# Kernel optimization log

Measured on AMD Instinct MI355X. Metric: run time of the kernel, lower is better.

The kernel has to match this reference:

```python
import jax, jax.numpy as jnp
import numpy as np

NUM_ITER = 5  # num_iterations
M, N, B = 972, 1944, 8  # check_matrix_row, check_matrix_column, unit_batch_size
ROW_DEG = 8  # check-node degree of the sparse parity matrix


def setup_inputs() -> dict:
    key = jax.random.key(0)
    # sparse binary parity-check matrix H (constant Tanner graph)
    rng = np.random.default_rng(0)
    H = np.zeros((M, N), np.float32)
    for i in range(M):
        H[i, rng.choice(N, ROW_DEG, replace=False)] = 1.0
    soft_input = 2.0 * jax.random.normal(key, (B, N), dtype=jnp.float32)  # channel LLRs
    check_weight = jnp.array([-1.07], dtype=jnp.float32)  # NMS init constant
    return {"soft_input": soft_input, "H": jnp.asarray(H), "check_weight": check_weight}


def _bp_iteration(cv, soft_input, H, check_weight):
    # ---- compute_vc (NMS: bit weight == 1.0) ----
    total = jnp.sum(cv, axis=1) + soft_input              # [B, N]
    vc = total[:, None, :] * H - cv                       # [B, M, N]
    # ---- compute_cv (min-sum branch) ----
    back = jnp.where(H == 0, -1e30 - 1.0, 0.0)[None]      # mask non-edges
    a = jnp.clip(jnp.abs(vc), 0.0, 1e30)
    dec = -a + back
    top2, _ = jax.lax.top_k(dec, 2)                       # [B, M, 2]
    min1 = (-top2[..., 0])[:, :, None] * H                # row min broadcast on edges
    min2 = (-top2[..., 1])[:, :, None] * H                # row second-min
    result = jnp.where(a > min1, min1, min2)              # exclude-self min
    sign_info = (1.0 - H)[None] + vc
    s = jnp.sign(sign_info)
    tot_sign = jnp.prod(s, axis=2)[:, :, None] * H
    result_sign = tot_sign * s                            # exclude-self sign product
    w = jax.nn.softplus(check_weight)                     # scalar NMS factor
    cv_new = result * jax.lax.stop_gradient(result_sign) * w
    return cv_new


def reference(soft_input, H, check_weight):
    Bn, n = soft_input.shape
    m = H.shape[0]
    cv0 = jnp.zeros((Bn, m, n), dtype=soft_input.dtype)

    def body(cv, _):
        return _bp_iteration(cv, soft_input, H, check_weight), None

    cv, _ = jax.lax.scan(body, cv0, None, length=NUM_ITER)
    # marginalize
    soft_output = jnp.sum(cv, axis=1) + soft_input
    return soft_output
```

## Files before the change

### kernel.cpp

```cpp
#include <hip/hip_runtime.h>
#include <math.h>

#define MM 972
#define NN 1944
#define BB 8
#define RD 8
#define NITER 5
#define MAXD 20
#define NEDGE (MM * RD)
#define DUMMY NEDGE

__global__ void build_adj(const float* __restrict__ H,
                          int* __restrict__ col_cnt,
                          int* __restrict__ row_cols,
                          int* __restrict__ col_edges) {
    const int m = blockIdx.x;
    __shared__ int cnt;
    if (threadIdx.x == 0) cnt = 0;
    __syncthreads();
    for (int n = threadIdx.x; n < NN; n += blockDim.x) {
        if (H[m * NN + n] != 0.0f) {
            int j = atomicAdd(&cnt, 1);
            row_cols[m * RD + j] = n;
            int k = atomicAdd(&col_cnt[n], 1);
            if (k < MAXD) col_edges[n * MAXD + k] = m * RD + j;
        }
    }
}

__global__ __launch_bounds__(1024, 1) void decode(const float* __restrict__ soft,
                                                  const float* __restrict__ cwp,
                                                  const int* __restrict__ col_cnt,
                                                  const int* __restrict__ row_cols,
                                                  const int* __restrict__ col_edges,
                                                  float* __restrict__ out) {
    __shared__ float cv_lds[NEDGE + 8];
    __shared__ float tot[NN];

    const int b = blockIdx.x;
    const int t = threadIdx.x;
    const float* soft_b = soft + b * NN;

    const float w = log1pf(expf(cwp[0]));

    const int n0 = t;
    const int n1 = t + 1024;
    const bool has1 = (n1 < NN);
    const float s0 = soft_b[n0];
    const float s1 = has1 ? soft_b[n1] : 0.0f;

    int e0[MAXD], e1[MAXD];
    {
        const int d0 = min(col_cnt[n0], MAXD);
        const int d1 = has1 ? min(col_cnt[n1], MAXD) : 0;
#pragma unroll
        for (int k = 0; k < MAXD; ++k) {
            e0[k] = (k < d0) ? col_edges[n0 * MAXD + k] : DUMMY;
            e1[k] = (k < d1) ? col_edges[n1 * MAXD + k] : DUMMY;
        }
    }

    int rc[RD];
    float cv[RD];
    if (t < MM) {
#pragma unroll
        for (int j = 0; j < RD; ++j) {
            rc[j] = row_cols[t * RD + j];
            cv[j] = 0.0f;
        }
    }

    tot[n0] = s0;
    if (has1) tot[n1] = s1;
    if (t == 0) {
#pragma unroll
        for (int k = 0; k < 8; ++k) cv_lds[NEDGE + k] = 0.0f;
    }
    __syncthreads();

    for (int it = 0; it < NITER; ++it) {
        if (t < MM) {
            float v[RD];
            float m1 = 3.0e38f, m2 = 3.0e38f, p = 1.0f;
#pragma unroll
            for (int j = 0; j < RD; ++j) {
                float vv = tot[rc[j]] - cv[j];
                v[j] = vv;
                float a = fminf(fabsf(vv), 1.0e30f);
                float s = (vv > 0.0f) ? 1.0f : ((vv < 0.0f) ? -1.0f : 0.0f);
                p *= s;
                if (a < m1) { m2 = m1; m1 = a; }
                else if (a < m2) { m2 = a; }
            }
#pragma unroll
            for (int j = 0; j < RD; ++j) {
                float a = fminf(fabsf(v[j]), 1.0e30f);
                float mag = (a > m1) ? m1 : m2;
                float s = (v[j] > 0.0f) ? 1.0f : ((v[j] < 0.0f) ? -1.0f : 0.0f);
                float nc = mag * (p * s) * w;
                cv[j] = nc;
                cv_lds[t * RD + j] = nc;
            }
        }
        __syncthreads();

        float a0 = 0.0f, a1 = 0.0f;
#pragma unroll
        for (int k = 0; k < MAXD; ++k) {
            a0 += cv_lds[e0[k]];
            a1 += cv_lds[e1[k]];
        }
        const float t0 = s0 + a0;
        const float t1 = s1 + a1;
        if (it == NITER - 1) {
            out[b * NN + n0] = t0;
            if (has1) out[b * NN + n1] = t1;
        } else {
            tot[n0] = t0;
            if (has1) tot[n1] = t1;
            __syncthreads();
        }
    }
}

extern "C" void kernel_launch(void* const* d_in, const int* in_sizes, int n_in,
                              void* d_out, int out_size, void* d_ws, size_t ws_size,
                              hipStream_t stream) {
    const float* soft = (const float*)d_in[0];
    const float* H    = (const float*)d_in[1];
    const float* cw   = (const float*)d_in[2];
    float* out = (float*)d_out;

    int* col_cnt   = (int*)d_ws;
    int* row_cols  = col_cnt + NN;
    int* col_edges = row_cols + MM * RD;

    hipMemsetAsync(col_cnt, 0, NN * sizeof(int), stream);
    build_adj<<<MM, 256, 0, stream>>>(H, col_cnt, row_cols, col_edges);
    decode<<<BB, 1024, 0, stream>>>(soft, cw, col_cnt, row_cols, col_edges, out);
}
```

Baseline: 87.04 us.

## Store check-to-variable messages in column-major padded slots for float4 gathers

Check nodes now scatter their messages into per-column slots (16 per variable node, with a rotating swizzle), so variable nodes sum their incoming messages with four float4 LDS loads instead of twenty scalar indexed gathers. This drops the per-column edge-index registers and the dummy-padded gather. The memset is replaced by a small zeroing kernel. LDS use grows to about 124 KB, and the scheme assumes column degree stays at or below 16; extra edges would collide in the last slot.

```diff
diff --git a/kernel.cpp b/kernel.cpp
--- a/kernel.cpp
+++ b/kernel.cpp
@@ -6,14 +6,17 @@
 #define BB 8
 #define RD 8
 #define NITER 5
-#define MAXD 20
-#define NEDGE (MM * RD)
-#define DUMMY NEDGE
+#define MAXD 16
+
+__global__ void zero_cnt(int* __restrict__ c) {
+    int i = blockIdx.x * blockDim.x + threadIdx.x;
+    if (i < NN) c[i] = 0;
+}
 
 __global__ void build_adj(const float* __restrict__ H,
                           int* __restrict__ col_cnt,
                           int* __restrict__ row_cols,
-                          int* __restrict__ col_edges) {
+                          int* __restrict__ row_slots) {
     const int m = blockIdx.x;
     __shared__ int cnt;
     if (threadIdx.x == 0) cnt = 0;
@@ -21,20 +24,21 @@
     for (int n = threadIdx.x; n < NN; n += blockDim.x) {
         if (H[m * NN + n] != 0.0f) {
             int j = atomicAdd(&cnt, 1);
-            row_cols[m * RD + j] = n;
             int k = atomicAdd(&col_cnt[n], 1);
-            if (k < MAXD) col_edges[n * MAXD + k] = m * RD + j;
+            if (k > MAXD - 1) k = MAXD - 1;
+            int phys = ((((k >> 2) + n) & 3) << 2) | (k & 3);
+            row_cols[m * RD + j]  = n;
+            row_slots[m * RD + j] = n * MAXD + phys;
         }
     }
 }
 
 __global__ __launch_bounds__(1024, 1) void decode(const float* __restrict__ soft,
                                                   const float* __restrict__ cwp,
-                                                  const int* __restrict__ col_cnt,
                                                   const int* __restrict__ row_cols,
-                                                  const int* __restrict__ col_edges,
+                                                  const int* __restrict__ row_slots,
                                                   float* __restrict__ out) {
-    __shared__ float cv_lds[NEDGE + 8];
+    __shared__ __align__(16) float cvc[NN * MAXD];
     __shared__ float tot[NN];
 
     const int b = blockIdx.x;
@@ -46,36 +50,29 @@
     const int n0 = t;
     const int n1 = t + 1024;
     const bool has1 = (n1 < NN);
+    const int n1c = has1 ? n1 : 0;
     const float s0 = soft_b[n0];
     const float s1 = has1 ? soft_b[n1] : 0.0f;
 
-    int e0[MAXD], e1[MAXD];
-    {
-        const int d0 = min(col_cnt[n0], MAXD);
-        const int d1 = has1 ? min(col_cnt[n1], MAXD) : 0;
-#pragma unroll
-        for (int k = 0; k < MAXD; ++k) {
-            e0[k] = (k < d0) ? col_edges[n0 * MAXD + k] : DUMMY;
-            e1[k] = (k < d1) ? col_edges[n1 * MAXD + k] : DUMMY;
-        }
-    }
-
-    int rc[RD];
+    int rc[RD], rs[RD];
     float cv[RD];
     if (t < MM) {
 #pragma unroll
         for (int j = 0; j < RD; ++j) {
             rc[j] = row_cols[t * RD + j];
+            rs[j] = row_slots[t * RD + j];
             cv[j] = 0.0f;
         }
     }
 
+    float4* cv4 = (float4*)cvc;
+#pragma unroll
+    for (int i = 0; i < 8; ++i) {
+        int idx = t + i * 1024;
+        if (idx < NN * MAXD / 4) cv4[idx] = make_float4(0.f, 0.f, 0.f, 0.f);
+    }
     tot[n0] = s0;
     if (has1) tot[n1] = s1;
-    if (t == 0) {
-#pragma unroll
-        for (int k = 0; k < 8; ++k) cv_lds[NEDGE + k] = 0.0f;
-    }
     __syncthreads();
 
     for (int it = 0; it < NITER; ++it) {
@@ -99,16 +96,18 @@
                 float s = (v[j] > 0.0f) ? 1.0f : ((v[j] < 0.0f) ? -1.0f : 0.0f);
                 float nc = mag * (p * s) * w;
                 cv[j] = nc;
-                cv_lds[t * RD + j] = nc;
+                cvc[rs[j]] = nc;
             }
         }
         __syncthreads();
 
         float a0 = 0.0f, a1 = 0.0f;
 #pragma unroll
-        for (int k = 0; k < MAXD; ++k) {
-            a0 += cv_lds[e0[k]];
-            a1 += cv_lds[e1[k]];
+        for (int i = 0; i < 4; ++i) {
+            float4 q0 = cv4[n0 * 4 + ((i + n0) & 3)];
+            a0 += (q0.x + q0.y) + (q0.z + q0.w);
+            float4 q1 = cv4[n1c * 4 + ((i + n1c) & 3)];
+            a1 += (q1.x + q1.y) + (q1.z + q1.w);
         }
         const float t0 = s0 + a0;
         const float t1 = s1 + a1;
@@ -133,9 +132,9 @@
 
     int* col_cnt   = (int*)d_ws;
     int* row_cols  = col_cnt + NN;
-    int* col_edges = row_cols + MM * RD;
+    int* row_slots = row_cols + MM * RD;
 
-    hipMemsetAsync(col_cnt, 0, NN * sizeof(int), stream);
-    build_adj<<<MM, 256, 0, stream>>>(H, col_cnt, row_cols, col_edges);
-    decode<<<BB, 1024, 0, stream>>>(soft, cw, col_cnt, row_cols, col_edges, out);
+    zero_cnt<<<2, 1024, 0, stream>>>(col_cnt);
+    build_adj<<<MM, 256, 0, stream>>>(H, col_cnt, row_cols, row_slots);
+    decode<<<BB, 1024, 0, stream>>>(soft, cw, row_cols, row_slots, out);
 }
```

Result: faster. 80.90 us (-7.1%).
